# Performance work log

Measured on AMD Instinct MI355X. Metric: run time of the kernel, lower is better.

## Reference

```python
import jax, jax.numpy as jnp
import numpy as np

NUM_HEADS = 16
KEY_DIM = 128
VALUE_DIM = 128
HIDDEN = 2048


def setup_inputs() -> dict:
    key = jax.random.key(0)
    k1, k2, k3 = jax.random.split(key, 3)
    B, T = 4, 2048
    hidden_states = jax.random.normal(k1, (B, T, HIDDEN), dtype=jnp.float32)
    # qkv_proj: Linear(hidden, H*(2*key_dim+value_dim)) no bias -> weight (out, in)
    qkv_out = NUM_HEADS * (2 * KEY_DIM + VALUE_DIM)
    w_qkv = jax.random.normal(k2, (qkv_out, HIDDEN), dtype=jnp.float32) * (1.0 / np.sqrt(HIDDEN))
    w_out = jax.random.normal(k3, (HIDDEN, NUM_HEADS * VALUE_DIM), dtype=jnp.float32) * (1.0 / np.sqrt(NUM_HEADS * VALUE_DIM))
    b_out = jnp.zeros((HIDDEN,), dtype=jnp.float32)
    return {"hidden_states": hidden_states, "w_qkv": w_qkv, "w_out": w_out, "b_out": b_out}


def reference(hidden_states, w_qkv, w_out, b_out):
    B, T, _ = hidden_states.shape
    H, Dk, Dv = NUM_HEADS, KEY_DIM, VALUE_DIM
    scale = 1.0 / np.sqrt(Dk).astype(np.float32)
    qkv = hidden_states @ w_qkv.T  # (B,T,H*(2Dk+Dv))
    q, k, v = jnp.split(qkv, [H * Dk, 2 * H * Dk], axis=-1)
    q = q.reshape(B, T, H, Dk).transpose(0, 2, 1, 3)  # (B,H,T,Dk)
    k = k.reshape(B, T, H, Dk).transpose(0, 2, 1, 3)
    v = v.reshape(B, T, H, Dv).transpose(0, 2, 1, 3)
    scores = jnp.einsum('bhtd,bhsd->bhts', q, k) * scale  # (B,H,T,S)
    causal = jnp.tril(jnp.ones((T, T), dtype=bool))
    scores = jnp.where(causal[None, None], scores, jnp.float32(-jnp.inf))
    attn = jax.nn.softmax(scores, axis=-1)
    out = jnp.einsum('bhts,bhsd->bhtd', attn, v)  # (B,H,T,Dv)
    out = out.transpose(0, 2, 1, 3).reshape(B, T, H * Dv)
    return out @ w_out.T + b_out
```

## Files before the change

kernel.cpp:

```cpp
#include <hip/hip_runtime.h>
#include <hip/hip_bf16.h>
#include <stdint.h>

#define HID   2048
#define NH    16
#define QKV_N 6144
#define BT    8192
#define TT    2048

typedef short bf16x8  __attribute__((ext_vector_type(8)));
typedef float f32x4   __attribute__((ext_vector_type(4)));
typedef float f32x16  __attribute__((ext_vector_type(16)));
typedef unsigned short u16;

__device__ __forceinline__ u16 f2bf(float f){
  union { float f; unsigned u; } v; v.f = f;
  unsigned r = 0x7fffu + ((v.u >> 16) & 1u);
  return (u16)((v.u + r) >> 16);
}
__device__ __forceinline__ float bf2f(u16 x){
  union { unsigned u; float f; } v; v.u = ((unsigned)x) << 16;
  return v.f;
}
__device__ __forceinline__ unsigned cvt_pk_bf16(float lo, float hi){
  unsigned r;
  asm("v_cvt_pk_bf16_f32 %0, %1, %2" : "=v"(r) : "v"(lo), "v"(hi));
  return r;
}

typedef __attribute__((address_space(3))) void lds_vt;
typedef const __attribute__((address_space(1))) void gbl_vt;

__device__ __forceinline__ void gload16(const void* g, void* l){
  __builtin_amdgcn_global_load_lds((gbl_vt*)g, (lds_vt*)l, 16, 0, 0);
}

#define FENCE() asm volatile("" ::: "memory")
#define SYNC()  { FENCE(); __builtin_amdgcn_s_barrier(); FENCE(); }

__global__ __launch_bounds__(256) void cvt_bf16(const float* __restrict__ in,
                                                u16* __restrict__ out, int n4){
  int i = blockIdx.x * blockDim.x + threadIdx.x;
  int stride = gridDim.x * blockDim.x;
  for (; i < n4; i += stride){
    float4 v = ((const float4*)in)[i];
    ushort4 o;
    o.x = f2bf(v.x); o.y = f2bf(v.y); o.z = f2bf(v.z); o.w = f2bf(v.w);
    ((ushort4*)out)[i] = o;
  }
}

template<int OUT_BF16>
__global__ __launch_bounds__(512, 2) void gemm256(const u16* __restrict__ A,
                                                  const u16* __restrict__ Bm,
                                                  u16* __restrict__ Cb,
                                                  float* __restrict__ Cf,
                                                  const float* __restrict__ bias,
                                                  int M, int N, int K)
{
  __shared__ u16 lds[4 * 256 * 64];
  u16* const Abuf[2] = { lds,          lds + 16384 };
  u16* const Bbuf[2] = { lds + 32768,  lds + 49152 };

  const int tid  = threadIdx.x;
  const int w    = tid >> 6;
  const int lane = tid & 63;
  const int wm   = w >> 2;
  const int wn   = w & 3;
  const int lr   = lane & 15;
  const int lg   = lane >> 4;

  int bid = blockIdx.x;
  { int qq = gridDim.x >> 3; bid = (bid & 7) * qq + (bid >> 3); }
  const int ntile = N >> 8;
  const int m0 = (bid / ntile) << 8;
  const int n0 = (bid % ntile) << 8;

  const int rS = tid >> 3;
  const int cS = ((tid & 7) ^ (rS & 7)) * 8;
  const u16* gA = A  + (size_t)(m0 + rS) * K + cS;
  const u16* gB = Bm + (size_t)(n0 + rS) * K + cS;
  const int wds = w * 512;

  f32x4 acc[8][4] = {};
  bf16x8 aq[2][2], bq[4][2];

  auto stgA = [&](int buf, int half, int kt){
    const u16* s = gA + (size_t)(half * 128) * K + (size_t)kt * 64;
    gload16(s,                  Abuf[buf] + half * 8192 + wds);
    gload16(s + (size_t)64 * K, Abuf[buf] + half * 8192 + 4096 + wds);
  };
  auto stgB = [&](int buf, int half, int kt){
    const u16* s = gB + (size_t)(half * 128) * K + (size_t)kt * 64;
    gload16(s,                  Bbuf[buf] + half * 8192 + wds);
    gload16(s + (size_t)64 * K, Bbuf[buf] + half * 8192 + 4096 + wds);
  };
  auto loadA = [&](const u16* ab, int q){
    #pragma unroll
    for (int kk = 0; kk < 2; ++kk){
      #pragma unroll
      for (int mf2 = 0; mf2 < 2; ++mf2){
        int row = wm * 128 + (q * 2 + mf2) * 16 + lr;
        int blk = (kk * 4 + lg) ^ (lr & 7);
        aq[mf2][kk] = *(const bf16x8*)(ab + row * 64 + blk * 8);
      }
    }
  };
  auto loadB = [&](const u16* bb){
    #pragma unroll
    for (int nf = 0; nf < 4; ++nf){
      #pragma unroll
      for (int kk = 0; kk < 2; ++kk){
        int row = wn * 64 + nf * 16 + lr;
        int blk = (kk * 4 + lg) ^ (lr & 7);
        bq[nf][kk] = *(const bf16x8*)(bb + row * 64 + blk * 8);
      }
    }
  };

#define MFMAQ(Q) do {                                                         \
    __builtin_amdgcn_s_setprio(1);                                            \
    _Pragma("unroll")                                                         \
    for (int kk = 0; kk < 2; ++kk){                                           \
      _Pragma("unroll")                                                       \
      for (int mf2 = 0; mf2 < 2; ++mf2){                                      \
        _Pragma("unroll")                                                     \
        for (int nf = 0; nf < 4; ++nf)                                        \
          acc[(Q)*2+mf2][nf] = __builtin_amdgcn_mfma_f32_16x16x32_bf16(       \
              aq[mf2][kk], bq[nf][kk], acc[(Q)*2+mf2][nf], 0, 0, 0);          \
      }                                                                       \
    }                                                                         \
    __builtin_amdgcn_s_setprio(0);                                            \
  } while (0)

  stgA(0, 0, 0); stgA(0, 1, 0);
  stgB(0, 0, 0); stgB(0, 1, 0);
  stgB(1, 0, 1); stgB(1, 1, 1);
  asm volatile("s_waitcnt vmcnt(4)" ::: "memory");
  SYNC();

  const int NI = K >> 7;
  for (int it = 0; it < NI; ++it){
    const int t = it * 2;
    const bool lastI = (it == NI - 1);

    loadB(Bbuf[0]);
    loadA(Abuf[0], 0);
    stgA(1, 0, t + 1);
    SYNC(); MFMAQ(0); SYNC();

    loadA(Abuf[0], 1);
    stgA(1, 1, t + 1);
    SYNC(); MFMAQ(1); SYNC();

    loadA(Abuf[0], 2);
    if (!lastI) stgB(0, 0, t + 2);
    SYNC(); MFMAQ(2); SYNC();

    loadA(Abuf[0], 3);
    if (!lastI) stgB(0, 1, t + 2);
    SYNC(); MFMAQ(3);
    if (lastI) asm volatile("s_waitcnt vmcnt(0)" ::: "memory");
    else       asm volatile("s_waitcnt vmcnt(4)" ::: "memory");
    SYNC();

    loadB(Bbuf[1]);
    loadA(Abuf[1], 0);
    if (!lastI) stgA(0, 0, t + 2);
    SYNC(); MFMAQ(0); SYNC();

    loadA(Abuf[1], 1);
    if (!lastI) stgA(0, 1, t + 2);
    SYNC(); MFMAQ(1); SYNC();

    loadA(Abuf[1], 2);
    if (!lastI) stgB(1, 0, t + 3);
    SYNC(); MFMAQ(2); SYNC();

    loadA(Abuf[1], 3);
    if (!lastI) stgB(1, 1, t + 3);
    SYNC(); MFMAQ(3);
    if (!lastI) asm volatile("s_waitcnt vmcnt(4)" ::: "memory");
    SYNC();
  }
#undef MFMAQ

  const int orow = m0 + wm * 128 + lg * 4;
  const int ocol = n0 + wn * 64 + lr;
  #pragma unroll
  for (int mf = 0; mf < 8; ++mf)
    #pragma unroll
    for (int nf = 0; nf < 4; ++nf)
      #pragma unroll
      for (int r = 0; r < 4; ++r){
        int row = orow + mf * 16 + r;
        int col = ocol + nf * 16;
        float v = acc[mf][nf][r];
        if (OUT_BF16)
          Cb[(size_t)row * N + col] = f2bf(v);
        else
          Cf[(size_t)row * N + col] = v + bias[col];
      }
}

__global__ __launch_bounds__(256) void vtrans(const u16* __restrict__ qkv,
                                              u16* __restrict__ vt2){
  __shared__ u16 tile[32][136];
  const int t5 = blockIdx.x;
  const int bh = blockIdx.y;
  const int b = bh >> 4, h = bh & 15;
  const int tid = threadIdx.x;

  #pragma unroll
  for (int p = 0; p < 2; ++p){
    int idx = p * 256 + tid;
    int row = idx >> 4;
    int c8  = (idx & 15) * 8;
    bf16x8 v = *(const bf16x8*)(qkv + (size_t)(b * TT + t5 * 32 + row) * QKV_N + 4096 + h * 128 + c8);
    *(bf16x8*)(&tile[row][c8]) = v;
  }
  __syncthreads();
  u16* outp = vt2 + (size_t)(bh * 64 + t5) * 4096;
  #pragma unroll
  for (int p = 0; p < 2; ++p){
    int id = p * 256 + tid;
    int r  = id >> 3;
    int sp = id & 7;
    int sl = sp ^ (r & 7);
    int d  = (sl >> 2) * 64 + r;
    int kv = (sl & 3) * 8;
    bf16x8 v;
    #pragma unroll
    for (int e = 0; e < 8; ++e) v[e] = (short)tile[kv + e][d];
    *(bf16x8*)(outp + id * 8) = v;
  }
}

__global__ __launch_bounds__(256, 3) void attn(const u16* __restrict__ qkv,
                                               const u16* __restrict__ vt2,
                                               u16* __restrict__ aout)
{
  __shared__ u16 Kl[3][32 * 128];
  __shared__ u16 Vl[3][64 * 64];

  const int qt = 15 - (int)blockIdx.y;
  const int bh = blockIdx.x;
  const int b = bh >> 4, h = bh & 15;
  const int tid  = threadIdx.x;
  const int w    = tid >> 6;
  const int lane = tid & 63;
  const int l31  = lane & 31;
  const int hi   = lane >> 5;
  const int sw7  = l31 & 7;

  const int qg = qt * 128 + w * 32 + l31;
  const float sc2 = 0.08838834764831845f * 1.4426950408889634f;

  bf16x8 qf[8];
  {
    const u16* qp = qkv + (size_t)(b * TT + qg) * QKV_N + h * 128 + hi * 8;
    #pragma unroll
    for (int s = 0; s < 8; ++s){
      bf16x8 raw = *(const bf16x8*)(qp + s * 16);
      unsigned pk[4];
      #pragma unroll
      for (int p2 = 0; p2 < 4; ++p2)
        pk[p2] = cvt_pk_bf16(bf2f((u16)raw[2 * p2]) * sc2,
                             bf2f((u16)raw[2 * p2 + 1]) * sc2);
      int4 u = { (int)pk[0], (int)pk[1], (int)pk[2], (int)pk[3] };
      qf[s] = *(bf16x8*)&u;
    }
  }

  f32x16 o[4] = {};
  float lsum = 0.f;

  const u16* ksrc = qkv + (size_t)(b * TT + (tid >> 4)) * QKV_N + 2048 + h * 128
                    + (((tid & 15) ^ ((tid >> 4) & 7)) * 8);
  const u16* vsrc = vt2 + (size_t)bh * (64 * 4096) + tid * 8;

  auto stage = [&](int buf, int j){
    const u16* ks = ksrc + (size_t)(j * 32) * QKV_N;
    gload16(ks,                      &Kl[buf][tid * 8]);
    gload16(ks + (size_t)16 * QKV_N, &Kl[buf][2048 + tid * 8]);
    const u16* vs = vsrc + (size_t)j * 4096;
    gload16(vs,        &Vl[buf][tid * 8]);
    gload16(vs + 2048, &Vl[buf][2048 + tid * 8]);
  };

  const int NT  = 4 * qt + 4;
  const int jme = qt * 4 + w;
  stage(0, 0);
  stage(1, 1);

  int cur = 0;
  for (int j = 0; j < NT; ++j){
    SYNC();
    if (j + 2 < NT){
      int nb = cur + 2; if (nb >= 3) nb -= 3;
      stage(nb, j + 2);
      asm volatile("s_waitcnt vmcnt(8)" ::: "memory");
    } else if (j + 1 < NT){
      asm volatile("s_waitcnt vmcnt(4)" ::: "memory");
    } else {
      asm volatile("s_waitcnt vmcnt(0)" ::: "memory");
    }
    SYNC();

    if (j <= jme){
      f32x16 s = {};
      const u16* KB = Kl[cur];
      __builtin_amdgcn_s_setprio(1);
      #pragma unroll
      for (int sl = 0; sl < 8; ++sl){
        const int sp = ((sl * 2 + hi) ^ sw7) * 8;
        bf16x8 kf = *(const bf16x8*)(KB + l31 * 128 + sp);
        s = __builtin_amdgcn_mfma_f32_32x32x16_bf16(kf, qf[sl], s, 0, 0, 0);
      }
      __builtin_amdgcn_s_setprio(0);

      if (j == jme){
        #pragma unroll
        for (int r = 0; r < 16; ++r){
          const int krow = (r & 3) + 8 * (r >> 2) + 4 * hi;
          if (krow > l31) s[r] = -3.0e38f;
        }
      }

      #pragma unroll
      for (int r = 0; r < 16; ++r) s[r] = exp2f(s[r]);
      {
        float t0 = (s[0] + s[1]) + (s[2] + s[3]);
        float t1 = (s[4] + s[5]) + (s[6] + s[7]);
        float t2 = (s[8] + s[9]) + (s[10] + s[11]);
        float t3 = (s[12] + s[13]) + (s[14] + s[15]);
        lsum += (t0 + t1) + (t2 + t3);
      }

      bf16x8 pf[2];
      #pragma unroll
      for (int kb = 0; kb < 2; ++kb){
        const int R0 = kb * 8;
        const unsigned wa0 = cvt_pk_bf16(s[R0],     s[R0 + 1]);
        const unsigned wa1 = cvt_pk_bf16(s[R0 + 2], s[R0 + 3]);
        const unsigned wb0 = cvt_pk_bf16(s[R0 + 4], s[R0 + 5]);
        const unsigned wb1 = cvt_pk_bf16(s[R0 + 6], s[R0 + 7]);
        const int s0 = hi ? (int)wa0 : (int)wb0;
        const int s1 = hi ? (int)wa1 : (int)wb1;
        const int r0 = __shfl_xor(s0, 32, 64);
        const int r1 = __shfl_xor(s1, 32, 64);
        int4 u;
        u.x = hi ? r0 : (int)wa0;
        u.y = hi ? r1 : (int)wa1;
        u.z = hi ? (int)wb0 : r0;
        u.w = hi ? (int)wb1 : r1;
        pf[kb] = *(bf16x8*)&u;
      }

      const u16* VB = Vl[cur];
      __builtin_amdgcn_s_setprio(1);
      #pragma unroll
      for (int db = 0; db < 4; ++db){
        const int r6 = (db & 1) * 32 + l31;
        const int hd = db >> 1;
        #pragma unroll
        for (int kb = 0; kb < 2; ++kb){
          const int sp = ((hd * 4 + kb * 2 + hi) ^ sw7) * 8;
          bf16x8 vf = *(const bf16x8*)(VB + r6 * 64 + sp);
          o[db] = __builtin_amdgcn_mfma_f32_32x32x16_bf16(vf, pf[kb], o[db], 0, 0, 0);
        }
      }
      __builtin_amdgcn_s_setprio(0);
    }

    ++cur; if (cur == 3) cur = 0;
  }

  const float lt = lsum + __shfl_xor(lsum, 32, 64);
  const float inv = 1.0f / lt;
  u16* op = aout + (size_t)(b * TT + qg) * HID + h * 128;
  #pragma unroll
  for (int db = 0; db < 4; ++db)
    #pragma unroll
    for (int rq = 0; rq < 4; ++rq){
      ushort4 pk;
      pk.x = f2bf(o[db][rq * 4 + 0] * inv);
      pk.y = f2bf(o[db][rq * 4 + 1] * inv);
      pk.z = f2bf(o[db][rq * 4 + 2] * inv);
      pk.w = f2bf(o[db][rq * 4 + 3] * inv);
      *(ushort4*)(op + db * 32 + rq * 8 + hi * 4) = pk;
    }
}

extern "C" void kernel_launch(void* const* d_in, const int* in_sizes, int n_in,
                              void* d_out, int out_size, void* d_ws, size_t ws_size,
                              hipStream_t stream)
{
  (void)in_sizes; (void)n_in; (void)out_size; (void)ws_size;
  const float* hs    = (const float*)d_in[0];
  const float* w_qkv = (const float*)d_in[1];
  const float* w_out = (const float*)d_in[2];
  const float* b_out = (const float*)d_in[3];
  float* out = (float*)d_out;

  char* ws = (char*)d_ws;
  u16* qkv_bf  = (u16*)(ws);
  u16* wout_bf = (u16*)(ws + 100663296);
  u16* hs_bf   = (u16*)(ws + 109051904);
  u16* attn_bf = hs_bf;
  u16* wqkv_bf = (u16*)(ws + 142606336);
  u16* vt2_bf  = wqkv_bf;

  cvt_bf16<<<2048, 256, 0, stream>>>(hs,    hs_bf,   (BT * HID) / 4);
  cvt_bf16<<<2048, 256, 0, stream>>>(w_qkv, wqkv_bf, (QKV_N * HID) / 4);
  cvt_bf16<<<1024, 256, 0, stream>>>(w_out, wout_bf, (HID * 2048) / 4);

  gemm256<1><<<(BT / 256) * (QKV_N / 256), 512, 0, stream>>>(
      hs_bf, wqkv_bf, qkv_bf, nullptr, nullptr, BT, QKV_N, HID);

  vtrans<<<dim3(TT / 32, 64), 256, 0, stream>>>(qkv_bf, vt2_bf);

  attn<<<dim3(64, 16), 256, 0, stream>>>(qkv_bf, vt2_bf, attn_bf);

  gemm256<0><<<(BT / 256) * (HID / 256), 512, 0, stream>>>(
      attn_bf, wout_bf, nullptr, out, b_out, BT, HID, HID);
}
```

Before: 389.2 us.

## Switch GEMM to 32x32x16 MFMA tiles and split attention QK accumulation chains

The projection GEMM moves from 16x16x32 MFMA fragments to 32x32x16 fragments. This halves the number of LDS fragment loads per FLOP and halves the sub-phases and barriers per k-tile, with global staging issued in larger groups. In the attention kernel, the QK^T dot product is split into two independent accumulator chains that are summed afterwards, shortening the MFMA dependency chain. The cost is extra registers, a different store pattern in the epilogue and 16 extra adds per tile.

```diff
diff --git a/kernel.cpp b/kernel.cpp
--- a/kernel.cpp
+++ b/kernel.cpp
@@ -67,8 +67,9 @@
   const int lane = tid & 63;
   const int wm   = w >> 2;
   const int wn   = w & 3;
-  const int lr   = lane & 15;
-  const int lg   = lane >> 4;
+  const int l31  = lane & 31;
+  const int hi   = lane >> 5;
+  const int sw7  = l31 & 7;
 
   int bid = blockIdx.x;
   { int qq = gridDim.x >> 3; bid = (bid & 7) * qq + (bid >> 3); }
@@ -82,8 +83,8 @@
   const u16* gB = Bm + (size_t)(n0 + rS) * K + cS;
   const int wds = w * 512;
 
-  f32x4 acc[8][4] = {};
-  bf16x8 aq[2][2], bq[4][2];
+  f32x16 acc[4][2] = {};
+  bf16x8 aq[2][4], bq[2][4];
 
   auto stgA = [&](int buf, int half, int kt){
     const u16* s = gA + (size_t)(half * 128) * K + (size_t)kt * 64;
@@ -95,39 +96,39 @@
     gload16(s,                  Bbuf[buf] + half * 8192 + wds);
     gload16(s + (size_t)64 * K, Bbuf[buf] + half * 8192 + 4096 + wds);
   };
-  auto loadA = [&](const u16* ab, int q){
-    #pragma unroll
-    for (int kk = 0; kk < 2; ++kk){
-      #pragma unroll
-      for (int mf2 = 0; mf2 < 2; ++mf2){
-        int row = wm * 128 + (q * 2 + mf2) * 16 + lr;
-        int blk = (kk * 4 + lg) ^ (lr & 7);
-        aq[mf2][kk] = *(const bf16x8*)(ab + row * 64 + blk * 8);
+  auto loadA = [&](const u16* ab, int mp){
+    #pragma unroll
+    for (int mi = 0; mi < 2; ++mi){
+      const int row = wm * 128 + (mp * 2 + mi) * 32 + l31;
+      #pragma unroll
+      for (int ks = 0; ks < 4; ++ks){
+        const int blk = (ks * 2 + hi) ^ sw7;
+        aq[mi][ks] = *(const bf16x8*)(ab + row * 64 + blk * 8);
       }
     }
   };
   auto loadB = [&](const u16* bb){
     #pragma unroll
-    for (int nf = 0; nf < 4; ++nf){
-      #pragma unroll
-      for (int kk = 0; kk < 2; ++kk){
-        int row = wn * 64 + nf * 16 + lr;
-        int blk = (kk * 4 + lg) ^ (lr & 7);
-        bq[nf][kk] = *(const bf16x8*)(bb + row * 64 + blk * 8);
+    for (int ni = 0; ni < 2; ++ni){
+      const int row = wn * 64 + ni * 32 + l31;
+      #pragma unroll
+      for (int ks = 0; ks < 4; ++ks){
+        const int blk = (ks * 2 + hi) ^ sw7;
+        bq[ni][ks] = *(const bf16x8*)(bb + row * 64 + blk * 8);
       }
     }
   };
 
-#define MFMAQ(Q) do {                                                         \
+#define MFMAP(MP) do {                                                        \
     __builtin_amdgcn_s_setprio(1);                                            \
     _Pragma("unroll")                                                         \
-    for (int kk = 0; kk < 2; ++kk){                                           \
+    for (int ks = 0; ks < 4; ++ks){                                           \
       _Pragma("unroll")                                                       \
-      for (int mf2 = 0; mf2 < 2; ++mf2){                                      \
+      for (int mi = 0; mi < 2; ++mi){                                         \
         _Pragma("unroll")                                                     \
-        for (int nf = 0; nf < 4; ++nf)                                        \
-          acc[(Q)*2+mf2][nf] = __builtin_amdgcn_mfma_f32_16x16x32_bf16(       \
-              aq[mf2][kk], bq[nf][kk], acc[(Q)*2+mf2][nf], 0, 0, 0);          \
+        for (int ni = 0; ni < 2; ++ni)                                        \
+          acc[(MP)*2+mi][ni] = __builtin_amdgcn_mfma_f32_32x32x16_bf16(       \
+              aq[mi][ks], bq[ni][ks], acc[(MP)*2+mi][ni], 0, 0, 0);           \
       }                                                                       \
     }                                                                         \
     __builtin_amdgcn_s_setprio(0);                                            \
@@ -146,61 +147,43 @@
 
     loadB(Bbuf[0]);
     loadA(Abuf[0], 0);
-    stgA(1, 0, t + 1);
-    SYNC(); MFMAQ(0); SYNC();
-
+    stgA(1, 0, t + 1); stgA(1, 1, t + 1);
+    SYNC(); MFMAP(0); SYNC();
     loadA(Abuf[0], 1);
-    stgA(1, 1, t + 1);
-    SYNC(); MFMAQ(1); SYNC();
-
-    loadA(Abuf[0], 2);
-    if (!lastI) stgB(0, 0, t + 2);
-    SYNC(); MFMAQ(2); SYNC();
-
-    loadA(Abuf[0], 3);
-    if (!lastI) stgB(0, 1, t + 2);
-    SYNC(); MFMAQ(3);
+    if (!lastI){ stgB(0, 0, t + 2); stgB(0, 1, t + 2); }
+    SYNC(); MFMAP(1);
     if (lastI) asm volatile("s_waitcnt vmcnt(0)" ::: "memory");
     else       asm volatile("s_waitcnt vmcnt(4)" ::: "memory");
     SYNC();
 
     loadB(Bbuf[1]);
     loadA(Abuf[1], 0);
-    if (!lastI) stgA(0, 0, t + 2);
-    SYNC(); MFMAQ(0); SYNC();
-
+    if (!lastI){ stgA(0, 0, t + 2); stgA(0, 1, t + 2); }
+    SYNC(); MFMAP(0); SYNC();
     loadA(Abuf[1], 1);
-    if (!lastI) stgA(0, 1, t + 2);
-    SYNC(); MFMAQ(1); SYNC();
-
-    loadA(Abuf[1], 2);
-    if (!lastI) stgB(1, 0, t + 3);
-    SYNC(); MFMAQ(2); SYNC();
-
-    loadA(Abuf[1], 3);
-    if (!lastI) stgB(1, 1, t + 3);
-    SYNC(); MFMAQ(3);
+    if (!lastI){ stgB(1, 0, t + 3); stgB(1, 1, t + 3); }
+    SYNC(); MFMAP(1);
     if (!lastI) asm volatile("s_waitcnt vmcnt(4)" ::: "memory");
     SYNC();
   }
-#undef MFMAQ
-
-  const int orow = m0 + wm * 128 + lg * 4;
-  const int ocol = n0 + wn * 64 + lr;
+#undef MFMAP
+
   #pragma unroll
-  for (int mf = 0; mf < 8; ++mf)
-    #pragma unroll
-    for (int nf = 0; nf < 4; ++nf)
-      #pragma unroll
-      for (int r = 0; r < 4; ++r){
-        int row = orow + mf * 16 + r;
-        int col = ocol + nf * 16;
-        float v = acc[mf][nf][r];
+  for (int mt = 0; mt < 4; ++mt)
+    #pragma unroll
+    for (int nt = 0; nt < 2; ++nt){
+      const int col = n0 + wn * 64 + nt * 32 + l31;
+      const float bs = OUT_BF16 ? 0.f : bias[col];
+      #pragma unroll
+      for (int r = 0; r < 16; ++r){
+        const int row = m0 + wm * 128 + mt * 32 + (r & 3) + 8 * (r >> 2) + 4 * hi;
+        const float v = acc[mt][nt][r];
         if (OUT_BF16)
           Cb[(size_t)row * N + col] = f2bf(v);
         else
-          Cf[(size_t)row * N + col] = v + bias[col];
-      }
+          Cf[(size_t)row * N + col] = v + bs;
+      }
+    }
 }
 
 __global__ __launch_bounds__(256) void vtrans(const u16* __restrict__ qkv,
@@ -308,16 +291,23 @@
     SYNC();
 
     if (j <= jme){
-      f32x16 s = {};
+      f32x16 sa = {}, sb = {};
       const u16* KB = Kl[cur];
       __builtin_amdgcn_s_setprio(1);
       #pragma unroll
-      for (int sl = 0; sl < 8; ++sl){
-        const int sp = ((sl * 2 + hi) ^ sw7) * 8;
-        bf16x8 kf = *(const bf16x8*)(KB + l31 * 128 + sp);
-        s = __builtin_amdgcn_mfma_f32_32x32x16_bf16(kf, qf[sl], s, 0, 0, 0);
+      for (int sl = 0; sl < 4; ++sl){
+        const int spa = ((sl * 2 + hi) ^ sw7) * 8;
+        const int spb = (((sl + 4) * 2 + hi) ^ sw7) * 8;
+        bf16x8 ka = *(const bf16x8*)(KB + l31 * 128 + spa);
+        bf16x8 kb2 = *(const bf16x8*)(KB + l31 * 128 + spb);
+        sa = __builtin_amdgcn_mfma_f32_32x32x16_bf16(ka,  qf[sl],     sa, 0, 0, 0);
+        sb = __builtin_amdgcn_mfma_f32_32x32x16_bf16(kb2, qf[sl + 4], sb, 0, 0, 0);
       }
       __builtin_amdgcn_s_setprio(0);
+
+      f32x16 s;
+      #pragma unroll
+      for (int r = 0; r < 16; ++r) s[r] = sa[r] + sb[r];
 
       if (j == jme){
         #pragma unroll
```

After: 406.0 us. 1.04x slower.
